# Optimization experiments

Hardware: AMD Instinct MI355X
Metric: run time of the kernel (lower is better)

The kernel has to match this reference:

```python
import jax, jax.numpy as jnp
import numpy as np

N_NODES = 20000
N_EDGES = 640000
NUM_FEATURES = 128
HIDDEN = 64
HEADS = 4
NUM_CLASSES = 16
NEG_SLOPE = 0.2  # PyG GATConv default leaky_relu slope


def gat_conv(x, src, dst, W, att_s, att_d, b, num_nodes, concat):
    """PyG-style GATConv (inference: attention dropout is identity).
    x: [N, F_in]; src/dst: [E] (self-loops already included);
    W: [F_in, H*C]; att_s/att_d: [H, C]; b: [H*C] or [C]."""
    H, C = att_s.shape
    h = (x @ W).reshape(num_nodes, H, C)            # [N,H,C]
    a_s = jnp.sum(h * att_s, axis=-1)               # [N,H]
    a_d = jnp.sum(h * att_d, axis=-1)               # [N,H]
    e = jax.nn.leaky_relu(a_s[src] + a_d[dst], NEG_SLOPE)  # [E,H]
    # softmax over incoming edges of each destination node
    emax = jax.ops.segment_max(e, dst, num_segments=num_nodes)  # [N,H]
    ex = jnp.exp(e - emax[dst])
    denom = jax.ops.segment_sum(ex, dst, num_segments=num_nodes)
    alpha = ex / denom[dst]                         # [E,H]
    msg = h[src] * alpha[..., None]                 # [E,H,C]
    out = jax.ops.segment_sum(msg, dst, num_segments=num_nodes)  # [N,H,C]
    out = out.reshape(num_nodes, H * C) if concat else out.mean(axis=1)
    return out + b


def setup_inputs() -> dict:
    key = jax.random.key(0)
    ks = jax.random.split(key, 12)
    d1_in, d1_out = NUM_FEATURES, HEADS * HIDDEN
    d2_in, d2_out = HEADS * HIDDEN, HEADS * HIDDEN
    return {
        "x": jax.random.normal(ks[0], (N_NODES, NUM_FEATURES), dtype=jnp.float32),
        "edge_index": jax.random.randint(ks[1], (2, N_EDGES), 0, N_NODES, dtype=jnp.int64)
        if jax.config.jax_enable_x64 else
        jax.random.randint(ks[1], (2, N_EDGES), 0, N_NODES, dtype=jnp.int32),
        "W1": jax.random.normal(ks[2], (d1_in, d1_out), dtype=jnp.float32) / np.sqrt(d1_in),
        "att_src1": jax.random.normal(ks[3], (HEADS, HIDDEN), dtype=jnp.float32) / np.sqrt(HIDDEN),
        "att_dst1": jax.random.normal(ks[4], (HEADS, HIDDEN), dtype=jnp.float32) / np.sqrt(HIDDEN),
        "b1": jnp.zeros((HEADS * HIDDEN,), dtype=jnp.float32),
        "W2": jax.random.normal(ks[5], (d2_in, d2_out), dtype=jnp.float32) / np.sqrt(d2_in),
        "att_src2": jax.random.normal(ks[6], (HEADS, HIDDEN), dtype=jnp.float32) / np.sqrt(HIDDEN),
        "att_dst2": jax.random.normal(ks[7], (HEADS, HIDDEN), dtype=jnp.float32) / np.sqrt(HIDDEN),
        "b2": jnp.zeros((HIDDEN,), dtype=jnp.float32),
        "Wout": jax.random.normal(ks[8], (HIDDEN, NUM_CLASSES), dtype=jnp.float32) / np.sqrt(HIDDEN),
        "bout": jnp.zeros((NUM_CLASSES,), dtype=jnp.float32),
    }


def reference(x, edge_index, W1, att_src1, att_dst1, b1, W2, att_src2, att_dst2, b2, Wout, bout):
    N = x.shape[0]
    loops = jnp.arange(N, dtype=edge_index.dtype)
    src = jnp.concatenate([edge_index[0], loops])   # PyG add_self_loops=True
    dst = jnp.concatenate([edge_index[1], loops])
    h = gat_conv(x, src, dst, W1, att_src1, att_dst1, b1, N, concat=True)
    h = jax.nn.elu(h)                               # dropout is identity at eval
    h = gat_conv(h, src, dst, W2, att_src2, att_dst2, b2, N, concat=False)
    return h @ Wout + bout
```

## Files before the change

### kernel.cpp

```cpp
#include <hip/hip_runtime.h>
#include <hip/hip_bf16.h>
#include <hip/hip_fp16.h>


#define HEADS 4
#define CDIM 64
#define HC 256
#define ELLW 96

typedef __attribute__((ext_vector_type(8))) short bf16x8;
typedef __attribute__((ext_vector_type(4))) float f32x4;

__device__ __forceinline__ short f32_to_bf16_rne(float v) {
  unsigned u = __float_as_uint(v);
  unsigned r = (u + 0x7FFFu + ((u >> 16) & 1u)) >> 16;
  return (short)r;
}
__device__ __forceinline__ float bf16_bits_to_f32(short s) {
  return __uint_as_float(((unsigned)(unsigned short)s) << 16);
}

__device__ __forceinline__ void fma_mix2(float& alo, float& ahi,
                                         unsigned reg, float ex) {
  asm("v_fma_mix_f32 %0, %2, %3, %0 op_sel:[0,0,0] op_sel_hi:[1,0,0]\n\t"
      "v_fma_mix_f32 %1, %2, %3, %1 op_sel:[1,0,0] op_sel_hi:[1,0,0]"
      : "+v"(alo), "+v"(ahi)
      : "v"(reg), "v"(ex));
}
__device__ __forceinline__ void fma_mix8(float ex, const uint4& u, float* acc) {
  fma_mix2(acc[0], acc[1], u.x, ex);
  fma_mix2(acc[2], acc[3], u.y, ex);
  fma_mix2(acc[4], acc[5], u.z, ex);
  fma_mix2(acc[6], acc[7], u.w, ex);
}

__global__ __launch_bounds__(256) void pack_w12_kernel(
    const float* __restrict__ W1, short* __restrict__ W1h,
    short* __restrict__ W1l, const float* __restrict__ W2,
    short* __restrict__ W2h, short* __restrict__ W2l) {
  const int i = blockIdx.x * 256 + threadIdx.x;
  if (i < 128 * 256) {
    const int k = i >> 8, n = i & 255;
    const float v = W1[i];
    const short hi = f32_to_bf16_rne(v);
    W1h[n * 128 + k] = hi;
    W1l[n * 128 + k] = f32_to_bf16_rne(v - bf16_bits_to_f32(hi));
  } else {
    const int j = i - 128 * 256;
    if (j >= 256 * 256) return;
    const int k = j >> 8, n = j & 255;
    const float v = W2[j];
    const short hi = f32_to_bf16_rne(v);
    W2h[n * 256 + k] = hi;
    W2l[n * 256 + k] = f32_to_bf16_rne(v - bf16_bits_to_f32(hi));
  }
}

__global__ __launch_bounds__(128) void gemm_mfma_split(
    const float* __restrict__ A, const short* __restrict__ Wt_hi,
    const short* __restrict__ Wt_lo, __half* __restrict__ h16,
    const float* __restrict__ att_s, const float* __restrict__ att_d,
    float* __restrict__ a_s, float* __restrict__ a_d, int M, int K) {
  __shared__ alignas(16) short As_hi[64 * 32];
  __shared__ alignas(16) short As_lo[64 * 32];
  const int t = threadIdx.x;
  const int wave = t >> 6;
  const int lane = t & 63;
  const int quad = lane >> 4;
  const int m16 = lane & 15;
  const int row0 = blockIdx.x * 64;
  const int col0 = blockIdx.y * 128 + wave * 64;
  const int head = col0 >> 6;

  f32x4 acc[4][4] = {};

  for (int k0 = 0; k0 < K; k0 += 32) {
    if (k0) __syncthreads();
#pragma unroll
    for (int uu = 0; uu < 2; ++uu) {
      const int u = t + uu * 128;
      const int r = u >> 2, seg = u & 3;
      const int gr = row0 + r;
      float vv[8] = {0.f, 0.f, 0.f, 0.f, 0.f, 0.f, 0.f, 0.f};
      if (gr < M) {
        const float* ap = A + (size_t)gr * K + k0 + seg * 8;
        const float4 v0 = *(const float4*)ap;
        const float4 v1 = *(const float4*)(ap + 4);
        vv[0] = v0.x; vv[1] = v0.y; vv[2] = v0.z; vv[3] = v0.w;
        vv[4] = v1.x; vv[5] = v1.y; vv[6] = v1.z; vv[7] = v1.w;
      }
      bf16x8 h8, l8;
#pragma unroll
      for (int j = 0; j < 8; ++j) {
        const short hi = f32_to_bf16_rne(vv[j]);
        h8[j] = hi;
        l8[j] = f32_to_bf16_rne(vv[j] - bf16_bits_to_f32(hi));
      }
      *(bf16x8*)(As_hi + r * 32 + seg * 8) = h8;
      *(bf16x8*)(As_lo + r * 32 + seg * 8) = l8;
    }
    bf16x8 b_hi[4], b_lo[4];
#pragma unroll
    for (int nt = 0; nt < 4; ++nt) {
      const size_t off = (size_t)(col0 + nt * 16 + m16) * K + k0 + quad * 8;
      b_hi[nt] = *(const bf16x8*)(Wt_hi + off);
      b_lo[nt] = *(const bf16x8*)(Wt_lo + off);
    }
    __syncthreads();
    bf16x8 a_hi[4], a_lo[4];
#pragma unroll
    for (int mt = 0; mt < 4; ++mt) {
      const int off = (mt * 16 + m16) * 32 + quad * 8;
      a_hi[mt] = *(const bf16x8*)(As_hi + off);
      a_lo[mt] = *(const bf16x8*)(As_lo + off);
    }
#pragma unroll
    for (int mt = 0; mt < 4; ++mt)
#pragma unroll
      for (int nt = 0; nt < 4; ++nt) {
        acc[mt][nt] = __builtin_amdgcn_mfma_f32_16x16x32_bf16(
            a_hi[mt], b_hi[nt], acc[mt][nt], 0, 0, 0);
        acc[mt][nt] = __builtin_amdgcn_mfma_f32_16x16x32_bf16(
            a_hi[mt], b_lo[nt], acc[mt][nt], 0, 0, 0);
        acc[mt][nt] = __builtin_amdgcn_mfma_f32_16x16x32_bf16(
            a_lo[mt], b_hi[nt], acc[mt][nt], 0, 0, 0);
      }
  }
  float sa[4], da[4];
#pragma unroll
  for (int nt = 0; nt < 4; ++nt) {
    sa[nt] = att_s[col0 + nt * 16 + m16];
    da[nt] = att_d[col0 + nt * 16 + m16];
  }
#pragma unroll
  for (int mt = 0; mt < 4; ++mt)
#pragma unroll
    for (int r = 0; r < 4; ++r) {
      const int gr = row0 + mt * 16 + quad * 4 + r;
      float ps = acc[mt][0][r] * sa[0] + acc[mt][1][r] * sa[1] +
                 acc[mt][2][r] * sa[2] + acc[mt][3][r] * sa[3];
      float pd = acc[mt][0][r] * da[0] + acc[mt][1][r] * da[1] +
                 acc[mt][2][r] * da[2] + acc[mt][3][r] * da[3];
#pragma unroll
      for (int off = 1; off <= 8; off <<= 1) {
        ps += __shfl_xor(ps, off);
        pd += __shfl_xor(pd, off);
      }
      if (gr < M) {
        if (m16 == 0) {
          a_s[gr * HEADS + head] = ps;
          a_d[gr * HEADS + head] = pd;
        }
#pragma unroll
        for (int nt = 0; nt < 4; ++nt)
          h16[(size_t)gr * HC + col0 + nt * 16 + m16] =
              __float2half(acc[mt][nt][r]);
      }
    }
}

__global__ __launch_bounds__(256) void ell_scatter_kernel(
    const int* __restrict__ src, const int* __restrict__ dst,
    int* __restrict__ cnt, int* __restrict__ ell, int E_raw, int Etot) {
  const int e = blockIdx.x * 256 + threadIdx.x;
  if (e >= Etot) return;
  const int s = (e < E_raw) ? src[e] : (e - E_raw);
  const int d = (e < E_raw) ? dst[e] : (e - E_raw);
  const int pos = atomicAdd(&cnt[d], 1);
  if (pos < ELLW) ell[d * ELLW + pos] = s;
}

__global__ __launch_bounds__(256) void gat_aggregate_kernel(
    const int* __restrict__ cnt, const int* __restrict__ ell,
    const __half* __restrict__ h16, const float* __restrict__ a_s,
    const float* __restrict__ a_d, const float* __restrict__ b,
    float* __restrict__ out, int mode) {
  const int bid = blockIdx.x;
  const int hd = bid & 3;
  const int n = (bid >> 2) * 4 + (threadIdx.x >> 6);
  const int lane = threadIdx.x & 63;
  const int q = lane >> 3;
  const int oc = lane & 7;
  const float ad = a_d[n * HEADS + hd];
  const int deg = cnt[n];
  const int* __restrict__ row = ell + n * ELLW;
  const char* hbase = (const char*)h16 + hd * 128 + oc * 16;
  const float* asb = a_s + hd;
  float acc[8] = {0.f, 0.f, 0.f, 0.f, 0.f, 0.f, 0.f, 0.f};
  float den = 0.f;
  int i = q;
  for (; i + 24 < deg; i += 32) {
    const int s0 = row[i];
    const int s1 = row[i + 8];
    const int s2 = row[i + 16];
    const int s3 = row[i + 24];
    const float as0 = asb[s0 * 4];
    const float as1 = asb[s1 * 4];
    const float as2 = asb[s2 * 4];
    const float as3 = asb[s3 * 4];
    const uint4 u0 = *(const uint4*)(hbase + ((unsigned)s0 << 9));
    const uint4 u1 = *(const uint4*)(hbase + ((unsigned)s1 << 9));
    const uint4 u2 = *(const uint4*)(hbase + ((unsigned)s2 << 9));
    const uint4 u3 = *(const uint4*)(hbase + ((unsigned)s3 << 9));
    float a0 = as0 + ad; a0 = fmaxf(a0, 0.2f * a0);
    float a1 = as1 + ad; a1 = fmaxf(a1, 0.2f * a1);
    float a2 = as2 + ad; a2 = fmaxf(a2, 0.2f * a2);
    float a3 = as3 + ad; a3 = fmaxf(a3, 0.2f * a3);
    const float e0 = __expf(a0);
    const float e1 = __expf(a1);
    const float e2 = __expf(a2);
    const float e3 = __expf(a3);
    den += e0 + e1 + e2 + e3;
    fma_mix8(e0, u0, acc);
    fma_mix8(e1, u1, acc);
    fma_mix8(e2, u2, acc);
    fma_mix8(e3, u3, acc);
  }
  for (; i + 8 < deg; i += 16) {
    const int s0 = row[i];
    const int s1 = row[i + 8];
    const float as0 = asb[s0 * 4];
    const float as1 = asb[s1 * 4];
    const uint4 u0 = *(const uint4*)(hbase + ((unsigned)s0 << 9));
    const uint4 u1 = *(const uint4*)(hbase + ((unsigned)s1 << 9));
    float a0 = as0 + ad; a0 = fmaxf(a0, 0.2f * a0);
    float a1 = as1 + ad; a1 = fmaxf(a1, 0.2f * a1);
    const float e0 = __expf(a0);
    const float e1 = __expf(a1);
    den += e0 + e1;
    fma_mix8(e0, u0, acc);
    fma_mix8(e1, u1, acc);
  }
  for (; i < deg; i += 8) {
    const int s = row[i];
    float a = asb[s * 4] + ad;
    a = fmaxf(a, 0.2f * a);
    const float ex = __expf(a);
    den += ex;
    const uint4 u = *(const uint4*)(hbase + ((unsigned)s << 9));
    fma_mix8(ex, u, acc);
  }
#pragma unroll
  for (int off = 8; off <= 32; off <<= 1) {
#pragma unroll
    for (int k = 0; k < 8; ++k) acc[k] += __shfl_xor(acc[k], off);
    den += __shfl_xor(den, off);
  }
  if (lane < 8) {
    const float inv = 1.f / den;
    float u[8];
#pragma unroll
    for (int k = 0; k < 8; ++k) u[k] = acc[k] * inv;
    if (mode == 0) {
      const float* bb = b + hd * CDIM + oc * 8;
#pragma unroll
      for (int k = 0; k < 8; ++k) {
        const float t0 = u[k] + bb[k];
        u[k] = (t0 > 0.f) ? t0 : (__expf(t0) - 1.f);
      }
    }
    float* op = out + (size_t)n * HC + hd * CDIM + oc * 8;
    *(float4*)op = make_float4(u[0], u[1], u[2], u[3]);
    *(float4*)(op + 4) = make_float4(u[4], u[5], u[6], u[7]);
  }
}

__global__ __launch_bounds__(256) void final_fused_kernel(
    const float* __restrict__ agg, const float* __restrict__ b2,
    const float* __restrict__ Wout, const float* __restrict__ bout,
    float* __restrict__ out, int N) {
  const int n = blockIdx.x * 4 + (threadIdx.x >> 6);
  const int c = threadIdx.x & 63;
  if (n >= N) return;
  const float* ar = agg + (size_t)n * HC;
  const float m = 0.25f * (ar[c] + ar[c + 64] + ar[c + 128] + ar[c + 192]) +
                  b2[c];
  const float4* wr = (const float4*)(Wout + c * 16);
  const float4 w0 = wr[0], w1 = wr[1], w2 = wr[2], w3 = wr[3];
  float p[16] = {m * w0.x, m * w0.y, m * w0.z, m * w0.w,
                 m * w1.x, m * w1.y, m * w1.z, m * w1.w,
                 m * w2.x, m * w2.y, m * w2.z, m * w2.w,
                 m * w3.x, m * w3.y, m * w3.z, m * w3.w};
#pragma unroll
  for (int off = 1; off < 64; off <<= 1)
#pragma unroll
    for (int j = 0; j < 16; ++j) p[j] += __shfl_xor(p[j], off);
  if (c == 0) {
    float* op = out + (size_t)n * 16;
    *(float4*)op = make_float4(p[0] + bout[0], p[1] + bout[1],
                               p[2] + bout[2], p[3] + bout[3]);
    *(float4*)(op + 4) = make_float4(p[4] + bout[4], p[5] + bout[5],
                                     p[6] + bout[6], p[7] + bout[7]);
    *(float4*)(op + 8) = make_float4(p[8] + bout[8], p[9] + bout[9],
                                     p[10] + bout[10], p[11] + bout[11]);
    *(float4*)(op + 12) = make_float4(p[12] + bout[12], p[13] + bout[13],
                                      p[14] + bout[14], p[15] + bout[15]);
  }
}

extern "C" void kernel_launch(void* const* d_in, const int* in_sizes, int n_in,
                              void* d_out, int out_size, void* d_ws, size_t ws_size,
                              hipStream_t stream) {
  const float* x      = (const float*)d_in[0];
  const int*   eidx   = (const int*)d_in[1];
  const float* W1     = (const float*)d_in[2];
  const float* att_s1 = (const float*)d_in[3];
  const float* att_d1 = (const float*)d_in[4];
  const float* b1     = (const float*)d_in[5];
  const float* W2     = (const float*)d_in[6];
  const float* att_s2 = (const float*)d_in[7];
  const float* att_d2 = (const float*)d_in[8];
  const float* b2     = (const float*)d_in[9];
  const float* Wout   = (const float*)d_in[10];
  const float* bout   = (const float*)d_in[11];
  float* out          = (float*)d_out;

  const int N     = in_sizes[0] / 128;
  const int E_raw = in_sizes[1] / 2;
  const int Etot  = E_raw + N;
  const int* src = eidx;
  const int* dst = eidx + E_raw;

  float* ws = (float*)d_ws;
  float* buf_agg = ws;
  float* buf_as  = buf_agg + (size_t)N * HC;
  float* buf_ad  = buf_as + (size_t)N * HEADS;
  __half* h16    = (__half*)(buf_ad + (size_t)N * HEADS);
  int* cnt  = (int*)(h16 + (size_t)N * HC);
  int* ell  = cnt + N;
  uintptr_t wp = ((uintptr_t)(ell + (size_t)N * ELLW) + 15) & ~(uintptr_t)15;
  short* wt1_hi = (short*)wp;
  short* wt1_lo = wt1_hi + 256 * 128;
  short* wt2_hi = wt1_lo + 256 * 128;
  short* wt2_lo = wt2_hi + 256 * 256;

  const dim3 blk(256);
  const int g_edge = (Etot + 255) / 256;
  const dim3 g_gemm((N + 63) / 64, 2);
  const dim3 blk_gemm(128);

  pack_w12_kernel<<<(384 * 256 + 255) / 256, blk, 0, stream>>>(
      W1, wt1_hi, wt1_lo, W2, wt2_hi, wt2_lo);
  hipMemsetAsync(cnt, 0, (size_t)N * sizeof(int), stream);
  ell_scatter_kernel<<<g_edge, blk, 0, stream>>>(src, dst, cnt, ell, E_raw, Etot);

  gemm_mfma_split<<<g_gemm, blk_gemm, 0, stream>>>(
      x, wt1_hi, wt1_lo, h16, att_s1, att_d1, buf_as, buf_ad, N, 128);
  gat_aggregate_kernel<<<N, blk, 0, stream>>>(cnt, ell, h16, buf_as,
                                              buf_ad, b1, buf_agg, 0);

  gemm_mfma_split<<<g_gemm, blk_gemm, 0, stream>>>(
      buf_agg, wt2_hi, wt2_lo, h16, att_s2, att_d2, buf_as, buf_ad, N, 256);
  gat_aggregate_kernel<<<N, blk, 0, stream>>>(cnt, ell, h16, buf_as,
                                              buf_ad, b2, buf_agg, 1);

  final_fused_kernel<<<(N + 3) / 4, blk, 0, stream>>>(buf_agg, b2, Wout, bout,
                                                      out, N);
}
```

Measured before the change: 270.9 us.

## Partition ELL scatter by destination group, pad counters, widen GEMM blocks

The edge scatter now splits edges into chunks and launches eight blocks per chunk. Each block handles only destinations in one of eight groups of 256-node ranges, which localises the atomic traffic. The per-node counters are padded to 16 ints apart to avoid contention on shared cache lines, and they are zeroed inside the pack kernel so the separate memset goes away. The GEMM now uses 256-thread blocks that cover all four heads, with one wave per head, replacing the two-column-block grid. In exchange, every edge's destination is read eight times and the counters take more workspace.

```diff
diff --git a/kernel.cpp b/kernel.cpp
--- a/kernel.cpp
+++ b/kernel.cpp
@@ -7,6 +7,8 @@
 #define CDIM 64
 #define HC 256
 #define ELLW 96
+#define CNTS 16
+#define NCHUNK 320
 
 typedef __attribute__((ext_vector_type(8))) short bf16x8;
 typedef __attribute__((ext_vector_type(4))) float f32x4;
@@ -37,8 +39,10 @@
 __global__ __launch_bounds__(256) void pack_w12_kernel(
     const float* __restrict__ W1, short* __restrict__ W1h,
     short* __restrict__ W1l, const float* __restrict__ W2,
-    short* __restrict__ W2h, short* __restrict__ W2l) {
+    short* __restrict__ W2h, short* __restrict__ W2l,
+    int* __restrict__ cnt, int N) {
   const int i = blockIdx.x * 256 + threadIdx.x;
+  if (i < N) cnt[i * CNTS] = 0;
   if (i < 128 * 256) {
     const int k = i >> 8, n = i & 255;
     const float v = W1[i];
@@ -56,7 +60,7 @@
   }
 }
 
-__global__ __launch_bounds__(128) void gemm_mfma_split(
+__global__ __launch_bounds__(256) void gemm_mfma_split(
     const float* __restrict__ A, const short* __restrict__ Wt_hi,
     const short* __restrict__ Wt_lo, __half* __restrict__ h16,
     const float* __restrict__ att_s, const float* __restrict__ att_d,
@@ -69,17 +73,15 @@
   const int quad = lane >> 4;
   const int m16 = lane & 15;
   const int row0 = blockIdx.x * 64;
-  const int col0 = blockIdx.y * 128 + wave * 64;
-  const int head = col0 >> 6;
+  const int col0 = wave * 64;
+  const int head = wave;
 
   f32x4 acc[4][4] = {};
 
   for (int k0 = 0; k0 < K; k0 += 32) {
     if (k0) __syncthreads();
-#pragma unroll
-    for (int uu = 0; uu < 2; ++uu) {
-      const int u = t + uu * 128;
-      const int r = u >> 2, seg = u & 3;
+    {
+      const int r = t >> 2, seg = t & 3;
       const int gr = row0 + r;
       float vv[8] = {0.f, 0.f, 0.f, 0.f, 0.f, 0.f, 0.f, 0.f};
       if (gr < M) {
@@ -161,13 +163,19 @@
 
 __global__ __launch_bounds__(256) void ell_scatter_kernel(
     const int* __restrict__ src, const int* __restrict__ dst,
-    int* __restrict__ cnt, int* __restrict__ ell, int E_raw, int Etot) {
-  const int e = blockIdx.x * 256 + threadIdx.x;
-  if (e >= Etot) return;
-  const int s = (e < E_raw) ? src[e] : (e - E_raw);
-  const int d = (e < E_raw) ? dst[e] : (e - E_raw);
-  const int pos = atomicAdd(&cnt[d], 1);
-  if (pos < ELLW) ell[d * ELLW + pos] = s;
+    int* __restrict__ cnt, int* __restrict__ ell, int E_raw, int Etot,
+    int chunk_sz) {
+  const int g = blockIdx.x & 7;
+  const int e0 = (blockIdx.x >> 3) * chunk_sz;
+  int e1 = e0 + chunk_sz;
+  if (e1 > Etot) e1 = Etot;
+  for (int e = e0 + threadIdx.x; e < e1; e += 256) {
+    const int d = (e < E_raw) ? dst[e] : (e - E_raw);
+    if (((d >> 8) & 7) != g) continue;
+    const int s = (e < E_raw) ? src[e] : (e - E_raw);
+    const int pos = atomicAdd(&cnt[d * CNTS], 1);
+    if (pos < ELLW) ell[d * ELLW + pos] = s;
+  }
 }
 
 __global__ __launch_bounds__(256) void gat_aggregate_kernel(
@@ -182,7 +190,7 @@
   const int q = lane >> 3;
   const int oc = lane & 7;
   const float ad = a_d[n * HEADS + hd];
-  const int deg = cnt[n];
+  const int deg = cnt[n * CNTS];
   const int* __restrict__ row = ell + n * ELLW;
   const char* hbase = (const char*)h16 + hd * 128 + oc * 16;
   const float* asb = a_s + hd;
@@ -327,7 +335,7 @@
   float* buf_ad  = buf_as + (size_t)N * HEADS;
   __half* h16    = (__half*)(buf_ad + (size_t)N * HEADS);
   int* cnt  = (int*)(h16 + (size_t)N * HC);
-  int* ell  = cnt + N;
+  int* ell  = cnt + (size_t)N * CNTS;
   uintptr_t wp = ((uintptr_t)(ell + (size_t)N * ELLW) + 15) & ~(uintptr_t)15;
   short* wt1_hi = (short*)wp;
   short* wt1_lo = wt1_hi + 256 * 128;
@@ -335,21 +343,20 @@
   short* wt2_lo = wt2_hi + 256 * 256;
 
   const dim3 blk(256);
-  const int g_edge = (Etot + 255) / 256;
-  const dim3 g_gemm((N + 63) / 64, 2);
-  const dim3 blk_gemm(128);
+  const int chunk_sz = (Etot + NCHUNK - 1) / NCHUNK;
+  const int g_gemm = (N + 63) / 64;
 
   pack_w12_kernel<<<(384 * 256 + 255) / 256, blk, 0, stream>>>(
-      W1, wt1_hi, wt1_lo, W2, wt2_hi, wt2_lo);
-  hipMemsetAsync(cnt, 0, (size_t)N * sizeof(int), stream);
-  ell_scatter_kernel<<<g_edge, blk, 0, stream>>>(src, dst, cnt, ell, E_raw, Etot);
-
-  gemm_mfma_split<<<g_gemm, blk_gemm, 0, stream>>>(
+      W1, wt1_hi, wt1_lo, W2, wt2_hi, wt2_lo, cnt, N);
+  ell_scatter_kernel<<<NCHUNK * 8, blk, 0, stream>>>(src, dst, cnt, ell,
+                                                     E_raw, Etot, chunk_sz);
+
+  gemm_mfma_split<<<g_gemm, blk, 0, stream>>>(
       x, wt1_hi, wt1_lo, h16, att_s1, att_d1, buf_as, buf_ad, N, 128);
   gat_aggregate_kernel<<<N, blk, 0, stream>>>(cnt, ell, h16, buf_as,
                                               buf_ad, b1, buf_agg, 0);
 
-  gemm_mfma_split<<<g_gemm, blk_gemm, 0, stream>>>(
+  gemm_mfma_split<<<g_gemm, blk, 0, stream>>>(
       buf_agg, wt2_hi, wt2_lo, h16, att_s2, att_d2, buf_as, buf_ad, N, 256);
   gat_aggregate_kernel<<<N, blk, 0, stream>>>(cnt, ell, h16, buf_as,
                                               buf_ad, b2, buf_agg, 1);
```

Result: faster. 256.6 us (-5.3%).
